# Kernel tuning notes

Hardware: AMD Instinct MI355X
Metric: run time of the kernel (lower is better)

The kernel has to match this reference:

```python
import jax, jax.numpy as jnp
import numpy as np

N_FIELDS = 8
HIDDEN = 128
GEO = 15
APP = 32
N_PTS = 524288


def setup_inputs() -> dict:
    key = jax.random.key(0)
    ks = jax.random.split(key, 12)
    cin = 3 + GEO + APP  # color-net input dim = 50
    s = 0.05
    return {
        "positions": jax.random.normal(ks[0], (N_PTS, 3), jnp.float32),
        "directions": jax.random.normal(ks[1], (N_PTS, 3), jnp.float32),
        "appearance_embedding": jax.random.normal(ks[2], (N_PTS, APP), jnp.float32),
        "centroids": jax.random.normal(ks[3], (N_FIELDS, 3), jnp.float32),
        "Wd1": jax.random.normal(ks[4], (N_FIELDS, 3, HIDDEN), jnp.float32) * s,
        "bd1": jnp.zeros((N_FIELDS, HIDDEN), jnp.float32),
        "Wd2": jax.random.normal(ks[5], (N_FIELDS, HIDDEN, 1 + GEO), jnp.float32) * s,
        "bd2": jnp.zeros((N_FIELDS, 1 + GEO), jnp.float32),
        "Wc1": jax.random.normal(ks[6], (N_FIELDS, cin, HIDDEN), jnp.float32) * s,
        "bc1": jnp.zeros((N_FIELDS, HIDDEN), jnp.float32),
        "Wc2": jax.random.normal(ks[7], (N_FIELDS, HIDDEN, 3), jnp.float32) * s,
        "bc2": jnp.zeros((N_FIELDS, 3), jnp.float32),
    }


def reference(positions, directions, appearance_embedding, centroids,
              Wd1, bd1, Wd2, bd2, Wc1, bc1, Wc2, bc2):
    # --- routing: nearest centroid (cdist + argmin); squared dist has same argmin ---
    d2 = jnp.sum((positions[:, None, :] - centroids[None, :, :]) ** 2, axis=-1)  # [N, F]
    assign = jnp.argmin(d2, axis=1)  # [N] int

    n = positions.shape[0]
    density = jnp.zeros((n, 1), positions.dtype)
    rgb = jnp.zeros((n, 3), positions.dtype)

    # dispatch/combine: masked dense evaluation per field (small fixed field count)
    for i in range(N_FIELDS):
        mask = (assign == i)[:, None]
        # field.density_fn: 2-layer MLP, trunc_exp density activation
        h = jax.nn.relu(positions @ Wd1[i] + bd1[i])          # [N, H]
        dout = h @ Wd2[i] + bd2[i]                            # [N, 1+GEO]
        dens_i = jnp.exp(dout[:, :1])                         # trunc_exp
        geo_i = dout[:, 1:]                                   # density embedding
        # field.get_outputs: color head on (dirs, geo_feat, appearance)
        cin = jnp.concatenate([directions, geo_i, appearance_embedding], axis=-1)
        hc = jax.nn.relu(cin @ Wc1[i] + bc1[i])               # [N, H]
        rgb_i = jax.nn.sigmoid(hc @ Wc2[i] + bc2[i])          # [N, 3]
        density = jnp.where(mask, dens_i, density)
        rgb = jnp.where(mask, rgb_i, rgb)

    # outputs concatenated: [density | rgb] -> [N, 4]
    return jnp.concatenate([density, rgb], axis=-1)
```

## Files before the change

kernel.cpp:

```cpp
#include <hip/hip_runtime.h>
#include <math.h>

#define NF 8
#define HID 128
#define TILE 576
#define NIT 9

typedef _Float16 f16;
typedef _Float16 h2 __attribute__((ext_vector_type(2)));
typedef _Float16 f16x8 __attribute__((ext_vector_type(8)));
typedef float f32x4 __attribute__((ext_vector_type(4)));
typedef unsigned int u32;
typedef u32 u32x2 __attribute__((ext_vector_type(2)));
typedef u32 u32x4 __attribute__((ext_vector_type(4)));

__device__ __forceinline__ u32 pk(float a, float b) {
    return __builtin_bit_cast(u32, __builtin_amdgcn_cvt_pkrtz(a, b));
}
__device__ __forceinline__ float dot2a(u32 a, u32 b, float c) {
    return __builtin_amdgcn_fdot2(__builtin_bit_cast(h2, a),
                                  __builtin_bit_cast(h2, b), c, false);
}


__device__ __forceinline__ int assign_field(float px, float py, float pz,
                                            const float* __restrict__ cen) {
    int best = 0;
    float bd = 3.4e38f;
#pragma unroll
    for (int k = 0; k < NF; ++k) {
        float dx = px - cen[k * 3 + 0];
        float dy = py - cen[k * 3 + 1];
        float dz = pz - cen[k * 3 + 2];
        float d = fmaf(dx, dx, fmaf(dy, dy, dz * dz));
        if (d < bd) { bd = d; best = k; }
    }
    return best;
}

__global__ void k_count(const float* __restrict__ pos, const float* __restrict__ cen,
                        int n, int* __restrict__ blockcnt) {
    __shared__ int lc[NF];
    int tid = threadIdx.x;
    if (tid < NF) lc[tid] = 0;
    __syncthreads();
    int i4 = blockIdx.x * blockDim.x + tid;
    int base = i4 * 4;
    if (base + 3 < n) {
        const float4* p4 = (const float4*)pos;
        float4 a = p4[i4 * 3 + 0];
        float4 b = p4[i4 * 3 + 1];
        float4 c = p4[i4 * 3 + 2];
        atomicAdd(&lc[assign_field(a.x, a.y, a.z, cen)], 1);
        atomicAdd(&lc[assign_field(a.w, b.x, b.y, cen)], 1);
        atomicAdd(&lc[assign_field(b.z, b.w, c.x, cen)], 1);
        atomicAdd(&lc[assign_field(c.y, c.z, c.w, cen)], 1);
    } else {
        for (int i = base; i < n; ++i)
            atomicAdd(&lc[assign_field(pos[3 * i], pos[3 * i + 1], pos[3 * i + 2], cen)], 1);
    }
    __syncthreads();
    if (tid < NF) blockcnt[blockIdx.x * NF + tid] = lc[tid];
}

__global__ void k_scatscan(const float* __restrict__ pos, const float* __restrict__ cen,
                           int n, int nb, int* __restrict__ ws) {
    const int tid = threadIdx.x;
    const int f = tid >> 6, lane = tid & 63;
    const int* c = ws + 32;
    int* perm = ws + 32 + nb * NF;
    __shared__ int totals[NF], pres[NF], starts[NF], cur[NF];

    int tot = 0, pre = 0;
    for (int b = lane; b < nb; b += 64) {
        int v = c[b * NF + f];
        tot += v;
        if (b < (int)blockIdx.x) pre += v;
    }
#pragma unroll
    for (int d = 1; d < 64; d <<= 1) {
        tot += __shfl_xor(tot, d, 64);
        pre += __shfl_xor(pre, d, 64);
    }
    if (lane == 0) { totals[f] = tot; pres[f] = pre; }
    __syncthreads();
    if (tid == 0) {
        int s = 0, tp = 0;
        for (int k = 0; k < NF; ++k) {
            starts[k] = s;
            if (blockIdx.x == 0) {
                ws[k] = totals[k];
                ws[8 + k] = s;
                ws[16 + k] = tp;
            }
            s += totals[k];
            tp += (totals[k] + TILE - 1) / TILE;
        }
        if (blockIdx.x == 0) ws[24] = tp;
    }
    __syncthreads();
    if (tid < NF) cur[tid] = starts[tid] + pres[tid];
    __syncthreads();

    int i4 = blockIdx.x * blockDim.x + tid;
    int base = i4 * 4;
    if (base + 3 < n) {
        const float4* p4 = (const float4*)pos;
        float4 a = p4[i4 * 3 + 0];
        float4 b = p4[i4 * 3 + 1];
        float4 cc = p4[i4 * 3 + 2];
        int f0 = assign_field(a.x, a.y, a.z, cen);
        int f1 = assign_field(a.w, b.x, b.y, cen);
        int f2 = assign_field(b.z, b.w, cc.x, cen);
        int f3 = assign_field(cc.y, cc.z, cc.w, cen);
        perm[atomicAdd(&cur[f0], 1)] = base;
        perm[atomicAdd(&cur[f1], 1)] = base + 1;
        perm[atomicAdd(&cur[f2], 1)] = base + 2;
        perm[atomicAdd(&cur[f3], 1)] = base + 3;
    } else {
        for (int i = base; i < n; ++i) {
            int ff = assign_field(pos[3 * i], pos[3 * i + 1], pos[3 * i + 2], cen);
            perm[atomicAdd(&cur[ff], 1)] = i;
        }
    }
}

__global__ __launch_bounds__(256, 3) void k_main(
    const float* __restrict__ positions, const float* __restrict__ directions,
    const float* __restrict__ app,
    const float* __restrict__ Wd1, const float* __restrict__ bd1,
    const float* __restrict__ Wd2, const float* __restrict__ bd2,
    const float* __restrict__ Wc1, const float* __restrict__ bc1,
    const float* __restrict__ Wc2, const float* __restrict__ bc2,
    const int* __restrict__ ws, int nb, float* __restrict__ out) {
    const int b = blockIdx.x;
    if (b >= ws[24]) return;
    int f = 0;
#pragma unroll
    for (int k = 1; k < NF; ++k) if (b >= ws[16 + k]) f = k;
    const int tile = b - ws[16 + f];
    const int cnt = ws[f];
    const int start = ws[8 + f];
    const int* perm = ws + 32 + nb * NF;
    const int tid = threadIdx.x;
    const int w = tid >> 6, lane = tid & 63;
    const int pt = lane & 15, quad = lane >> 4;

    __shared__ __align__(16) f16 sWc1t[HID * 72];
    __shared__ __align__(16) u32 sWc2p[64 * 4];
    __shared__ __align__(16) int sIdx[4][16];
    __shared__ __align__(16) u32x2 sDir[4][16];
    __shared__ __align__(16) f16 sGeo[4][16][16];
    __shared__ __align__(16) f16 sH[4][16 * 136];

    if (tid < HID) {
        int h = tid;
        f16* row = &sWc1t[h * 72];
        const float* Wf = Wc1 + f * 50 * HID;
        row[0] = (f16)Wf[0 * HID + h];
        row[1] = (f16)Wf[1 * HID + h];
        row[2] = (f16)Wf[2 * HID + h];
        row[3] = (f16)bc1[f * HID + h];
        row[4] = 0; row[5] = 0; row[6] = 0; row[7] = 0;
        for (int a = 0; a < 32; ++a) row[8 + a] = (f16)Wf[(18 + a) * HID + h];
        for (int g = 0; g < 15; ++g) row[40 + g] = (f16)Wf[(3 + g) * HID + h];
        for (int z = 55; z < 72; ++z) row[z] = 0;
    }
    if (tid >= 128 && tid < 192) {
        int hp = tid - 128;
        const float* W2 = Wc2 + f * HID * 3;
        sWc2p[hp * 4 + 0] = pk(W2[(2 * hp) * 3 + 0], W2[(2 * hp + 1) * 3 + 0]);
        sWc2p[hp * 4 + 1] = pk(W2[(2 * hp) * 3 + 1], W2[(2 * hp + 1) * 3 + 1]);
        sWc2p[hp * 4 + 2] = pk(W2[(2 * hp) * 3 + 2], W2[(2 * hp + 1) * 3 + 2]);
        sWc2p[hp * 4 + 3] = 0;
    }
    if (lane < 16) sGeo[w][pt][15] = (f16)0.f;

    u32 wd1a0[8], wd1a1[8];
    if (quad == 0) {
        const float* W1 = Wd1 + f * 3 * HID;
        const float* B1 = bd1 + f * HID;
#pragma unroll
        for (int mt = 0; mt < 8; ++mt) {
            int m = 16 * mt + pt;
            wd1a0[mt] = pk(W1[m], W1[HID + m]);
            wd1a1[mt] = pk(W1[2 * HID + m], B1[m]);
        }
    } else {
#pragma unroll
        for (int mt = 0; mt < 8; ++mt) { wd1a0[mt] = 0; wd1a1[mt] = 0; }
    }
    f16x8 wd2b[4];
    {
        const float* W2d = Wd2 + f * HID * 16;
#pragma unroll
        for (int s = 0; s < 4; ++s) {
            u32x4 v;
#pragma unroll
            for (int jp = 0; jp < 4; ++jp) {
                int k = quad * 8 + 32 * s + 2 * jp;
                v[jp] = pk(W2d[k * 16 + pt], W2d[(k + 1) * 16 + pt]);
            }
            wd2b[s] = __builtin_bit_cast(f16x8, v);
        }
    }
    const float bd2v = bd2[f * 16 + pt];
    const float c20 = bc2[f * 3 + 0], c21 = bc2[f * 3 + 1], c22 = bc2[f * 3 + 2];
    __syncthreads();

    const int tstart = tile * TILE;
    const int cidx = (quad == 0) ? 3 : (quad - 1);

    int g_idx;
    float4 g_c0, g_c1;
    float g_p0, g_p1, g_p2;
    {
        int plc = tstart + w * 16 + pt;
        if (plc > cnt - 1) plc = cnt - 1;
        g_idx = perm[start + plc];
        const float4* ap = (const float4*)(app + g_idx * 32 + cidx * 8);
        g_c0 = ap[0]; g_c1 = ap[1];
        if (quad == 0) {
            g_p0 = positions[g_idx * 3 + 0];
            g_p1 = positions[g_idx * 3 + 1];
            g_p2 = positions[g_idx * 3 + 2];
        } else if (quad == 1) {
            g_p0 = directions[g_idx * 3 + 0];
            g_p1 = directions[g_idx * 3 + 1];
            g_p2 = directions[g_idx * 3 + 2];
        }
    }

#pragma unroll 1
    for (int it = 0; it < NIT; ++it) {
        const int pbase = tstart + it * 64 + w * 16;
        if (pbase >= cnt) break;

        const int cur_idx = g_idx;
        const float4 cur_c0 = g_c0, cur_c1 = g_c1;
        const float cp0 = g_p0, cp1 = g_p1, cp2 = g_p2;
        if (quad == 0) {
            sIdx[w][pt] = cur_idx;
        } else if (quad == 1) {
            u32x2 d2; d2.x = pk(cp0, cp1); d2.y = pk(cp2, 1.f);
            sDir[w][pt] = d2;
        }

        {
            const int nbase = tstart + (it + 1) * 64 + w * 16;
            if (it + 1 < NIT && nbase < cnt) {
                int plc = nbase + pt;
                if (plc > cnt - 1) plc = cnt - 1;
                g_idx = perm[start + plc];
                const float4* ap = (const float4*)(app + g_idx * 32 + cidx * 8);
                g_c0 = ap[0]; g_c1 = ap[1];
                if (quad == 0) {
                    g_p0 = positions[g_idx * 3 + 0];
                    g_p1 = positions[g_idx * 3 + 1];
                    g_p2 = positions[g_idx * 3 + 2];
                } else if (quad == 1) {
                    g_p0 = directions[g_idx * 3 + 0];
                    g_p1 = directions[g_idx * 3 + 1];
                    g_p2 = directions[g_idx * 3 + 2];
                }
            }
        }

        u32x4 xv;
        xv.x = (quad == 0) ? pk(cp0, cp1) : 0u;
        xv.y = (quad == 0) ? pk(cp2, 1.f) : 0u;
        xv.z = 0u; xv.w = 0u;
        const f16x8 xb = __builtin_bit_cast(f16x8, xv);
#pragma unroll
        for (int mt = 0; mt < 8; ++mt) {
            u32x4 av; av.x = wd1a0[mt]; av.y = wd1a1[mt]; av.z = 0u; av.w = 0u;
            f16x8 af = __builtin_bit_cast(f16x8, av);
            f32x4 acc = {0.f, 0.f, 0.f, 0.f};
            acc = __builtin_amdgcn_mfma_f32_16x16x32_f16(af, xb, acc, 0, 0, 0);
            u32x2 hw;
            hw.x = pk(fmaxf(acc[0], 0.f), fmaxf(acc[1], 0.f));
            hw.y = pk(fmaxf(acc[2], 0.f), fmaxf(acc[3], 0.f));
            *(u32x2*)&sH[w][pt * 136 + 16 * mt + quad * 4] = hw;
        }

        f32x4 dacc = {bd2v, bd2v, bd2v, bd2v};
#pragma unroll
        for (int s = 0; s < 4; ++s) {
            f16x8 ha = __builtin_bit_cast(f16x8,
                *(const u32x4*)&sH[w][pt * 136 + quad * 8 + 32 * s]);
            dacc = __builtin_amdgcn_mfma_f32_16x16x32_f16(ha, wd2b[s], dacc, 0, 0, 0);
        }
        if (pt == 0) {
            int4 si = *(const int4*)&sIdx[w][quad * 4];
            out[si.x * 4] = __expf(dacc[0]);
            out[si.y * 4] = __expf(dacc[1]);
            out[si.z * 4] = __expf(dacc[2]);
            out[si.w * 4] = __expf(dacc[3]);
        } else {
#pragma unroll
            for (int r = 0; r < 4; ++r)
                sGeo[w][quad * 4 + r][pt - 1] = (f16)dacc[r];
        }

        u32x4 capp;
        capp.x = pk(cur_c0.x, cur_c0.y); capp.y = pk(cur_c0.z, cur_c0.w);
        capp.z = pk(cur_c1.x, cur_c1.y); capp.w = pk(cur_c1.z, cur_c1.w);
        f16x8 cb0, cb1;
        {
            u32x4 t0 = capp;
            if (quad == 0) {
                u32x2 d2 = sDir[w][pt];
                t0.x = d2.x; t0.y = d2.y; t0.z = 0u; t0.w = 0u;
            }
            cb0 = __builtin_bit_cast(f16x8, t0);
            u32x4 t1;
            if (quad == 0) t1 = capp;
            else if (quad == 3) { t1.x = 0u; t1.y = 0u; t1.z = 0u; t1.w = 0u; }
            else t1 = *(const u32x4*)&sGeo[w][pt][(quad - 1) * 8];
            cb1 = __builtin_bit_cast(f16x8, t1);
        }
        float r0 = 0.f, r1 = 0.f, r2 = 0.f;
#pragma unroll
        for (int mt = 0; mt < 8; ++mt) {
            f16x8 wa0 = __builtin_bit_cast(f16x8,
                *(const u32x4*)&sWc1t[(16 * mt + pt) * 72 + quad * 8]);
            f16x8 wa1 = __builtin_bit_cast(f16x8,
                *(const u32x4*)&sWc1t[(16 * mt + pt) * 72 + quad * 8 + 32]);
            f32x4 cacc = {0.f, 0.f, 0.f, 0.f};
            cacc = __builtin_amdgcn_mfma_f32_16x16x32_f16(wa0, cb0, cacc, 0, 0, 0);
            cacc = __builtin_amdgcn_mfma_f32_16x16x32_f16(wa1, cb1, cacc, 0, 0, 0);
            u32 h01 = pk(fmaxf(cacc[0], 0.f), fmaxf(cacc[1], 0.f));
            u32 h23 = pk(fmaxf(cacc[2], 0.f), fmaxf(cacc[3], 0.f));
            u32x4 w01 = *(const u32x4*)&sWc2p[(8 * mt + 2 * quad) * 4];
            u32x4 w23 = *(const u32x4*)&sWc2p[(8 * mt + 2 * quad + 1) * 4];
            r0 = dot2a(h01, w01.x, r0); r0 = dot2a(h23, w23.x, r0);
            r1 = dot2a(h01, w01.y, r1); r1 = dot2a(h23, w23.y, r1);
            r2 = dot2a(h01, w01.z, r2); r2 = dot2a(h23, w23.z, r2);
        }
        r0 += __shfl_xor(r0, 16, 64); r0 += __shfl_xor(r0, 32, 64);
        r1 += __shfl_xor(r1, 16, 64); r1 += __shfl_xor(r1, 32, 64);
        r2 += __shfl_xor(r2, 16, 64); r2 += __shfl_xor(r2, 32, 64);
        if (quad == 0) {
            float s0 = 1.f / (1.f + __expf(-(r0 + c20)));
            float s1 = 1.f / (1.f + __expf(-(r1 + c21)));
            float s2 = 1.f / (1.f + __expf(-(r2 + c22)));
            out[cur_idx * 4 + 1] = s0;
            *(float2*)&out[cur_idx * 4 + 2] = make_float2(s1, s2);
        }
    }
}

extern "C" void kernel_launch(void* const* d_in, const int* in_sizes, int n_in,
                              void* d_out, int out_size, void* d_ws, size_t ws_size,
                              hipStream_t stream) {
    const float* positions = (const float*)d_in[0];
    const float* directions = (const float*)d_in[1];
    const float* app = (const float*)d_in[2];
    const float* centroids = (const float*)d_in[3];
    const float* Wd1 = (const float*)d_in[4];
    const float* bd1 = (const float*)d_in[5];
    const float* Wd2 = (const float*)d_in[6];
    const float* bd2 = (const float*)d_in[7];
    const float* Wc1 = (const float*)d_in[8];
    const float* bc1 = (const float*)d_in[9];
    const float* Wc2 = (const float*)d_in[10];
    const float* bc2 = (const float*)d_in[11];
    float* out = (float*)d_out;
    int* wsi = (int*)d_ws;
    const int n = in_sizes[0] / 3;
    const int nb = (n + 2047) / 2048;
    const int max_tiles = (n + TILE - 1) / TILE + NF;

    k_count<<<nb, 512, 0, stream>>>(positions, centroids, n, wsi + 32);
    k_scatscan<<<nb, 512, 0, stream>>>(positions, centroids, n, nb, wsi);
    k_main<<<max_tiles, 256, 0, stream>>>(positions, directions, app, Wd1, bd1, Wd2,
                                          bd2, Wc1, bc1, Wc2, bc2, wsi, nb, out);
}
```

Before: 60.48 us.

## Software-pipeline main loop with two-deep gather prefetch and skewed MLP stages

Replaces the single-buffered loop with a manually unrolled two-stage pipeline. The gathers for point batches now run two iterations ahead in alternating A/B register sets. The density first layer for the next batch is interleaved with the second-layer and color-head work of the current batch. The goal is to hide global gather latency and LDS round trips behind MFMA work, at the cost of more live registers under the 256x3 launch bound, which risks spills.

```diff
diff --git a/kernel.cpp b/kernel.cpp
--- a/kernel.cpp
+++ b/kernel.cpp
@@ -125,6 +125,121 @@
     }
 }
 
+#define GATH(IT, IDX, C0, C1, P0, P1, P2)                                     \
+    {                                                                         \
+        if ((IT) < NIT) {                                                     \
+            int _plc = tstart + (IT) * 64 + w * 16 + pt;                      \
+            if (_plc > cnt - 1) _plc = cnt - 1;                               \
+            IDX = perm[start + _plc];                                         \
+            const float4* _ap = (const float4*)(app + IDX * 32 + cidx * 8);   \
+            C0 = _ap[0]; C1 = _ap[1];                                         \
+            if (quad == 0) {                                                  \
+                P0 = positions[IDX * 3 + 0];                                  \
+                P1 = positions[IDX * 3 + 1];                                  \
+                P2 = positions[IDX * 3 + 2];                                  \
+            } else if (quad == 1) {                                           \
+                P0 = directions[IDX * 3 + 0];                                 \
+                P1 = directions[IDX * 3 + 1];                                 \
+                P2 = directions[IDX * 3 + 2];                                 \
+            }                                                                 \
+        }                                                                     \
+    }
+
+#define BODY(AI, AC0, AC1, AP0, AP1, AP2, BI, BC0, BC1, BP0, BP1, BP2, IT)    \
+    {                                                                         \
+        f32x4 dacc = {bd2v, bd2v, bd2v, bd2v};                                \
+        _Pragma("unroll")                                                     \
+        for (int s = 0; s < 4; ++s) {                                         \
+            f16x8 ha = __builtin_bit_cast(f16x8,                              \
+                *(const u32x4*)&sH[w][pt * 136 + quad * 8 + 32 * s]);         \
+            dacc = __builtin_amdgcn_mfma_f32_16x16x32_f16(ha, wd2b[s], dacc, 0, 0, 0); \
+        }                                                                     \
+        if (pt == 0) {                                                        \
+            int4 si = *(const int4*)&sIdx[w][quad * 4];                       \
+            out[si.x * 4] = __expf(dacc[0]);                                  \
+            out[si.y * 4] = __expf(dacc[1]);                                  \
+            out[si.z * 4] = __expf(dacc[2]);                                  \
+            out[si.w * 4] = __expf(dacc[3]);                                  \
+        } else {                                                              \
+            _Pragma("unroll")                                                 \
+            for (int r = 0; r < 4; ++r)                                       \
+                sGeo[w][quad * 4 + r][pt - 1] = (f16)dacc[r];                 \
+        }                                                                     \
+        const int cidx_s = AI;                                                \
+        u32x4 capp;                                                           \
+        capp.x = pk(AC0.x, AC0.y); capp.y = pk(AC0.z, AC0.w);                 \
+        capp.z = pk(AC1.x, AC1.y); capp.w = pk(AC1.z, AC1.w);                 \
+        f16x8 cb0, cb1;                                                       \
+        {                                                                     \
+            u32x4 t0 = capp;                                                  \
+            if (quad == 0) {                                                  \
+                u32x2 d2 = sDir[w][pt];                                       \
+                t0.x = d2.x; t0.y = d2.y; t0.z = 0u; t0.w = 0u;               \
+            }                                                                 \
+            cb0 = __builtin_bit_cast(f16x8, t0);                              \
+            u32x4 t1;                                                         \
+            if (quad == 0) t1 = capp;                                         \
+            else if (quad == 3) { t1.x = 0u; t1.y = 0u; t1.z = 0u; t1.w = 0u; } \
+            else t1 = *(const u32x4*)&sGeo[w][pt][(quad - 1) * 8];            \
+            cb1 = __builtin_bit_cast(f16x8, t1);                              \
+        }                                                                     \
+        if (quad == 0) sIdx[w][pt] = BI;                                      \
+        else if (quad == 1) {                                                 \
+            u32x2 d2; d2.x = pk(BP0, BP1); d2.y = pk(BP2, 1.f);               \
+            sDir[w][pt] = d2;                                                 \
+        }                                                                     \
+        GATH((IT) + 2, AI, AC0, AC1, AP0, AP1, AP2);                          \
+                      \
+        {                                                                     \
+            u32x4 xv;                                                         \
+            xv.x = (quad == 0) ? pk(BP0, BP1) : 0u;                           \
+            xv.y = (quad == 0) ? pk(BP2, 1.f) : 0u;                           \
+            xv.z = 0u; xv.w = 0u;                                             \
+            const f16x8 xb = __builtin_bit_cast(f16x8, xv);                   \
+            _Pragma("unroll")                                                 \
+            for (int mt = 0; mt < 8; ++mt) {                                  \
+                u32x4 av; av.x = wd1a0[mt]; av.y = wd1a1[mt];                 \
+                av.z = 0u; av.w = 0u;                                         \
+                f16x8 af = __builtin_bit_cast(f16x8, av);                     \
+                f32x4 acc = {0.f, 0.f, 0.f, 0.f};                             \
+                acc = __builtin_amdgcn_mfma_f32_16x16x32_f16(af, xb, acc, 0, 0, 0); \
+                u32x2 hw;                                                     \
+                hw.x = pk(fmaxf(acc[0], 0.f), fmaxf(acc[1], 0.f));            \
+                hw.y = pk(fmaxf(acc[2], 0.f), fmaxf(acc[3], 0.f));            \
+                *(u32x2*)&sH[w][pt * 136 + 16 * mt + quad * 4] = hw;          \
+            }                                                                 \
+        }                                                                     \
+                                                 \
+        float r0 = 0.f, r1 = 0.f, r2 = 0.f;                                   \
+        _Pragma("unroll")                                                     \
+        for (int mt = 0; mt < 8; ++mt) {                                      \
+            f16x8 wa0 = __builtin_bit_cast(f16x8,                             \
+                *(const u32x4*)&sWc1t[(16 * mt + pt) * 72 + quad * 8]);       \
+            f16x8 wa1 = __builtin_bit_cast(f16x8,                             \
+                *(const u32x4*)&sWc1t[(16 * mt + pt) * 72 + quad * 8 + 32]);  \
+            f32x4 cacc = {0.f, 0.f, 0.f, 0.f};                                \
+            cacc = __builtin_amdgcn_mfma_f32_16x16x32_f16(wa0, cb0, cacc, 0, 0, 0); \
+            cacc = __builtin_amdgcn_mfma_f32_16x16x32_f16(wa1, cb1, cacc, 0, 0, 0); \
+            u32 h01 = pk(fmaxf(cacc[0], 0.f), fmaxf(cacc[1], 0.f));           \
+            u32 h23 = pk(fmaxf(cacc[2], 0.f), fmaxf(cacc[3], 0.f));           \
+            u32x4 w01 = *(const u32x4*)&sWc2p[(8 * mt + 2 * quad) * 4];       \
+            u32x4 w23 = *(const u32x4*)&sWc2p[(8 * mt + 2 * quad + 1) * 4];   \
+            r0 = dot2a(h01, w01.x, r0); r0 = dot2a(h23, w23.x, r0);           \
+            r1 = dot2a(h01, w01.y, r1); r1 = dot2a(h23, w23.y, r1);           \
+            r2 = dot2a(h01, w01.z, r2); r2 = dot2a(h23, w23.z, r2);           \
+        }                                                                     \
+        r0 += __shfl_xor(r0, 16, 64); r0 += __shfl_xor(r0, 32, 64);           \
+        r1 += __shfl_xor(r1, 16, 64); r1 += __shfl_xor(r1, 32, 64);           \
+        r2 += __shfl_xor(r2, 16, 64); r2 += __shfl_xor(r2, 32, 64);           \
+        if (quad == 0) {                                                      \
+            float s0 = 1.f / (1.f + __expf(-(r0 + c20)));                     \
+            float s1 = 1.f / (1.f + __expf(-(r1 + c21)));                     \
+            float s2 = 1.f / (1.f + __expf(-(r2 + c22)));                     \
+            out[cidx_s * 4 + 1] = s0;                                         \
+            *(float2*)&out[cidx_s * 4 + 2] = make_float2(s1, s2);             \
+        }                                                                     \
+    }
+
 __global__ __launch_bounds__(256, 3) void k_main(
     const float* __restrict__ positions, const float* __restrict__ directions,
     const float* __restrict__ app,
@@ -211,64 +326,22 @@
     const int tstart = tile * TILE;
     const int cidx = (quad == 0) ? 3 : (quad - 1);
 
-    int g_idx;
-    float4 g_c0, g_c1;
-    float g_p0, g_p1, g_p2;
+    int iA = 0, iB = 0;
+    float4 cA0 = {}, cA1 = {}, cB0 = {}, cB1 = {};
+    float pA0 = 0.f, pA1 = 0.f, pA2 = 0.f;
+    float pB0 = 0.f, pB1 = 0.f, pB2 = 0.f;
+    GATH(0, iA, cA0, cA1, pA0, pA1, pA2);
+    GATH(1, iB, cB0, cB1, pB0, pB1, pB2);
+
+    if (quad == 0) sIdx[w][pt] = iA;
+    else if (quad == 1) {
+        u32x2 d2; d2.x = pk(pA0, pA1); d2.y = pk(pA2, 1.f);
+        sDir[w][pt] = d2;
+    }
     {
-        int plc = tstart + w * 16 + pt;
-        if (plc > cnt - 1) plc = cnt - 1;
-        g_idx = perm[start + plc];
-        const float4* ap = (const float4*)(app + g_idx * 32 + cidx * 8);
-        g_c0 = ap[0]; g_c1 = ap[1];
-        if (quad == 0) {
-            g_p0 = positions[g_idx * 3 + 0];
-            g_p1 = positions[g_idx * 3 + 1];
-            g_p2 = positions[g_idx * 3 + 2];
-        } else if (quad == 1) {
-            g_p0 = directions[g_idx * 3 + 0];
-            g_p1 = directions[g_idx * 3 + 1];
-            g_p2 = directions[g_idx * 3 + 2];
-        }
-    }
-
-#pragma unroll 1
-    for (int it = 0; it < NIT; ++it) {
-        const int pbase = tstart + it * 64 + w * 16;
-        if (pbase >= cnt) break;
-
-        const int cur_idx = g_idx;
-        const float4 cur_c0 = g_c0, cur_c1 = g_c1;
-        const float cp0 = g_p0, cp1 = g_p1, cp2 = g_p2;
-        if (quad == 0) {
-            sIdx[w][pt] = cur_idx;
-        } else if (quad == 1) {
-            u32x2 d2; d2.x = pk(cp0, cp1); d2.y = pk(cp2, 1.f);
-            sDir[w][pt] = d2;
-        }
-
-        {
-            const int nbase = tstart + (it + 1) * 64 + w * 16;
-            if (it + 1 < NIT && nbase < cnt) {
-                int plc = nbase + pt;
-                if (plc > cnt - 1) plc = cnt - 1;
-                g_idx = perm[start + plc];
-                const float4* ap = (const float4*)(app + g_idx * 32 + cidx * 8);
-                g_c0 = ap[0]; g_c1 = ap[1];
-                if (quad == 0) {
-                    g_p0 = positions[g_idx * 3 + 0];
-                    g_p1 = positions[g_idx * 3 + 1];
-                    g_p2 = positions[g_idx * 3 + 2];
-                } else if (quad == 1) {
-                    g_p0 = directions[g_idx * 3 + 0];
-                    g_p1 = directions[g_idx * 3 + 1];
-                    g_p2 = directions[g_idx * 3 + 2];
-                }
-            }
-        }
-
         u32x4 xv;
-        xv.x = (quad == 0) ? pk(cp0, cp1) : 0u;
-        xv.y = (quad == 0) ? pk(cp2, 1.f) : 0u;
+        xv.x = (quad == 0) ? pk(pA0, pA1) : 0u;
+        xv.y = (quad == 0) ? pk(pA2, 1.f) : 0u;
         xv.z = 0u; xv.w = 0u;
         const f16x8 xb = __builtin_bit_cast(f16x8, xv);
 #pragma unroll
@@ -282,72 +355,19 @@
             hw.y = pk(fmaxf(acc[2], 0.f), fmaxf(acc[3], 0.f));
             *(u32x2*)&sH[w][pt * 136 + 16 * mt + quad * 4] = hw;
         }
-
-        f32x4 dacc = {bd2v, bd2v, bd2v, bd2v};
-#pragma unroll
-        for (int s = 0; s < 4; ++s) {
-            f16x8 ha = __builtin_bit_cast(f16x8,
-                *(const u32x4*)&sH[w][pt * 136 + quad * 8 + 32 * s]);
-            dacc = __builtin_amdgcn_mfma_f32_16x16x32_f16(ha, wd2b[s], dacc, 0, 0, 0);
-        }
-        if (pt == 0) {
-            int4 si = *(const int4*)&sIdx[w][quad * 4];
-            out[si.x * 4] = __expf(dacc[0]);
-            out[si.y * 4] = __expf(dacc[1]);
-            out[si.z * 4] = __expf(dacc[2]);
-            out[si.w * 4] = __expf(dacc[3]);
-        } else {
-#pragma unroll
-            for (int r = 0; r < 4; ++r)
-                sGeo[w][quad * 4 + r][pt - 1] = (f16)dacc[r];
-        }
-
-        u32x4 capp;
-        capp.x = pk(cur_c0.x, cur_c0.y); capp.y = pk(cur_c0.z, cur_c0.w);
-        capp.z = pk(cur_c1.x, cur_c1.y); capp.w = pk(cur_c1.z, cur_c1.w);
-        f16x8 cb0, cb1;
-        {
-            u32x4 t0 = capp;
-            if (quad == 0) {
-                u32x2 d2 = sDir[w][pt];
-                t0.x = d2.x; t0.y = d2.y; t0.z = 0u; t0.w = 0u;
-            }
-            cb0 = __builtin_bit_cast(f16x8, t0);
-            u32x4 t1;
-            if (quad == 0) t1 = capp;
-            else if (quad == 3) { t1.x = 0u; t1.y = 0u; t1.z = 0u; t1.w = 0u; }
-            else t1 = *(const u32x4*)&sGeo[w][pt][(quad - 1) * 8];
-            cb1 = __builtin_bit_cast(f16x8, t1);
-        }
-        float r0 = 0.f, r1 = 0.f, r2 = 0.f;
-#pragma unroll
-        for (int mt = 0; mt < 8; ++mt) {
-            f16x8 wa0 = __builtin_bit_cast(f16x8,
-                *(const u32x4*)&sWc1t[(16 * mt + pt) * 72 + quad * 8]);
-            f16x8 wa1 = __builtin_bit_cast(f16x8,
-                *(const u32x4*)&sWc1t[(16 * mt + pt) * 72 + quad * 8 + 32]);
-            f32x4 cacc = {0.f, 0.f, 0.f, 0.f};
-            cacc = __builtin_amdgcn_mfma_f32_16x16x32_f16(wa0, cb0, cacc, 0, 0, 0);
-            cacc = __builtin_amdgcn_mfma_f32_16x16x32_f16(wa1, cb1, cacc, 0, 0, 0);
-            u32 h01 = pk(fmaxf(cacc[0], 0.f), fmaxf(cacc[1], 0.f));
-            u32 h23 = pk(fmaxf(cacc[2], 0.f), fmaxf(cacc[3], 0.f));
-            u32x4 w01 = *(const u32x4*)&sWc2p[(8 * mt + 2 * quad) * 4];
-            u32x4 w23 = *(const u32x4*)&sWc2p[(8 * mt + 2 * quad + 1) * 4];
-            r0 = dot2a(h01, w01.x, r0); r0 = dot2a(h23, w23.x, r0);
-            r1 = dot2a(h01, w01.y, r1); r1 = dot2a(h23, w23.y, r1);
-            r2 = dot2a(h01, w01.z, r2); r2 = dot2a(h23, w23.z, r2);
-        }
-        r0 += __shfl_xor(r0, 16, 64); r0 += __shfl_xor(r0, 32, 64);
-        r1 += __shfl_xor(r1, 16, 64); r1 += __shfl_xor(r1, 32, 64);
-        r2 += __shfl_xor(r2, 16, 64); r2 += __shfl_xor(r2, 32, 64);
-        if (quad == 0) {
-            float s0 = 1.f / (1.f + __expf(-(r0 + c20)));
-            float s1 = 1.f / (1.f + __expf(-(r1 + c21)));
-            float s2 = 1.f / (1.f + __expf(-(r2 + c22)));
-            out[cur_idx * 4 + 1] = s0;
-            *(float2*)&out[cur_idx * 4 + 2] = make_float2(s1, s2);
-        }
-    }
+    }
+
+#pragma unroll 1
+    for (int it = 0; it + 1 < NIT; it += 2) {
+        if (tstart + it * 64 + w * 16 >= cnt) goto done;
+        BODY(iA, cA0, cA1, pA0, pA1, pA2, iB, cB0, cB1, pB0, pB1, pB2, it);
+        if (tstart + (it + 1) * 64 + w * 16 >= cnt) goto done;
+        BODY(iB, cB0, cB1, pB0, pB1, pB2, iA, cA0, cA1, pA0, pA1, pA2, it + 1);
+    }
+    if (tstart + (NIT - 1) * 64 + w * 16 < cnt) {
+        BODY(iA, cA0, cA1, pA0, pA1, pA2, iB, cB0, cB1, pB0, pB1, pB2, NIT - 1);
+    }
+done:;
 }
 
 extern "C" void kernel_launch(void* const* d_in, const int* in_sizes, int n_in,
```

Result: no change. 60.66 us (+0.3%).
